# Optimization experiments

Hardware: AMD Instinct MI355X
Metric: run time of the kernel (lower is better)

The kernel has to match this reference:

```python
import jax, jax.numpy as jnp
import numpy as np

D_MODEL = 768
D_FF = 2048
N_EXP = 8
TOP_K = 2


def setup_inputs() -> dict:
    key = jax.random.key(0)
    ks = jax.random.split(key, 8)
    s = 0.02
    inputs = jax.random.normal(ks[0], (4, 2048, D_MODEL), dtype=jnp.float32)
    gate_w = jax.random.normal(ks[1], (D_MODEL, N_EXP), dtype=jnp.float32) * s
    w1 = jax.random.normal(ks[2], (N_EXP, D_MODEL, D_FF), dtype=jnp.float32) * s
    w3 = jax.random.normal(ks[3], (N_EXP, D_MODEL, D_FF), dtype=jnp.float32) * s
    w2 = jax.random.normal(ks[4], (N_EXP, D_FF, D_MODEL), dtype=jnp.float32) * s
    sw1 = jax.random.normal(ks[5], (D_MODEL, D_FF), dtype=jnp.float32) * s
    sw3 = jax.random.normal(ks[6], (D_MODEL, D_FF), dtype=jnp.float32) * s
    sw2 = jax.random.normal(ks[7], (D_FF, D_MODEL), dtype=jnp.float32) * s
    return {"inputs": inputs, "gate_w": gate_w, "w1": w1, "w3": w3, "w2": w2,
            "sw1": sw1, "sw3": sw3, "sw2": sw2}


def _swiglu(x, wa, wb, wc):
    # silu(x @ wa) * (x @ wb) @ wc
    return (jax.nn.silu(x @ wa) * (x @ wb)) @ wc


def reference(inputs, gate_w, w1, w3, w2, sw1, sw3, sw2):
    B, T, D = inputs.shape
    x = inputs.reshape(-1, D)                      # [N, D], N = B*T
    logits = x @ gate_w                            # [N, E]
    topk_scores, topk_idx = jax.lax.top_k(logits, TOP_K)  # [N, K]
    probs = jax.nn.softmax(topk_scores.astype(jnp.float32), axis=-1).astype(inputs.dtype)
    # per-token per-expert combine weight: [N, E]
    one_hot = jax.nn.one_hot(topk_idx, N_EXP, dtype=probs.dtype)  # [N, K, E]
    comb = jnp.einsum('nk,nke->ne', probs, one_hot)               # [N, E]
    out = jnp.zeros_like(x)
    for e in range(N_EXP):  # fixed small expert loop
        out = out + comb[:, e:e + 1] * _swiglu(x, w1[e], w3[e], w2[e])
    out = out + _swiglu(x, sw1, sw3, sw2)
    return out.reshape(B, T, D)
```

## Files before the change

### kernel.cpp

```cpp
#include <hip/hip_runtime.h>
#include <hip/hip_bf16.h>

#define N_TOK 8192
#define DM 768
#define DFF 2048
#define NE 8
#define SHARED_BASE 17408
#define TOTAL_ROWS 25600

typedef __attribute__((ext_vector_type(8))) __bf16 bf16x8;
typedef __attribute__((ext_vector_type(4))) float f32x4;

__device__ __forceinline__ unsigned short f2bf(float f) {
  union { float f; unsigned u; } a; a.f = f;
  unsigned r = a.u + 0x7FFFu + ((a.u >> 16) & 1u);
  return (unsigned short)(r >> 16);
}

__device__ __forceinline__ float bfu(unsigned short u) {
  union { unsigned u; float f; } x; x.u = (unsigned)u << 16; return x.f;
}

__device__ __forceinline__ void gload16(const void* g, void* l) {
  __builtin_amdgcn_global_load_lds((const __attribute__((address_space(1))) void*)g,
                                   (__attribute__((address_space(3))) void*)l, 16, 0, 0);
}


__global__ void transpose_all_kernel(
    const float* __restrict__ w1, const float* __restrict__ w3, const float* __restrict__ w2,
    const float* __restrict__ sw1, const float* __restrict__ sw3, const float* __restrict__ sw2,
    unsigned short* __restrict__ w1T, unsigned short* __restrict__ w3T,
    unsigned short* __restrict__ w2T,
    unsigned short* __restrict__ sw1T, unsigned short* __restrict__ sw3T,
    unsigned short* __restrict__ sw2T) {
  __shared__ float tile[64][65];
  const int z = blockIdx.z;
  const float* s; unsigned short* d; int R, C;
  if (z < 8)       { s = w1 + (size_t)z * DM * DFF;        d = w1T + (size_t)z * DM * DFF;        R = DM;  C = DFF; }
  else if (z < 16) { s = w3 + (size_t)(z - 8) * DM * DFF;  d = w3T + (size_t)(z - 8) * DM * DFF;  R = DM;  C = DFF; }
  else if (z < 24) { s = w2 + (size_t)(z - 16) * DFF * DM; d = w2T + (size_t)(z - 16) * DFF * DM; R = DFF; C = DM;  }
  else if (z == 24){ s = sw1; d = sw1T; R = DM;  C = DFF; }
  else if (z == 25){ s = sw3; d = sw3T; R = DM;  C = DFF; }
  else             { s = sw2; d = sw2T; R = DFF; C = DM;  }
  int c0 = blockIdx.x * 64, r0 = blockIdx.y * 64;
  if (c0 >= C || r0 >= R) return;
  int tx = threadIdx.x & 63, ty = threadIdx.x >> 6;
#pragma unroll
  for (int i = 0; i < 16; i++) {
    int row = i * 4 + ty;
    tile[row][tx] = s[(size_t)(r0 + row) * C + c0 + tx];
  }
  __syncthreads();
  int tx2 = threadIdx.x & 31, ty8 = threadIdx.x >> 5;
#pragma unroll
  for (int i = 0; i < 8; i++) {
    int row = i * 8 + ty8;
    ushort2 v;
    v.x = f2bf(tile[tx2 * 2][row]);
    v.y = f2bf(tile[tx2 * 2 + 1][row]);
    *(ushort2*)&d[(size_t)(c0 + row) * R + r0 + tx2 * 2] = v;
  }
}

__global__ __launch_bounds__(256) void gate_kernel(
    const float* __restrict__ x, const float* __restrict__ gw,
    float* __restrict__ probs, int* __restrict__ idxo, unsigned short* __restrict__ xb) {
  __shared__ float gws[8][768];
  const int tid = threadIdx.x;
  for (int i = tid; i < DM * 2; i += 256) {
    float4 v = ((const float4*)gw)[i];
    int dd = i >> 1;
    int e0 = (i & 1) * 4;
    gws[e0 + 0][dd] = v.x; gws[e0 + 1][dd] = v.y;
    gws[e0 + 2][dd] = v.z; gws[e0 + 3][dd] = v.w;
  }
  __syncthreads();
  const int lane = tid & 63, wv = tid >> 6;
  const int tok0 = blockIdx.x * 16 + wv * 4;
  for (int i = 0; i < 4; i++) {
    const int n = tok0 + i;
    const float* xr = x + (size_t)n * DM;
    float xv[12];
#pragma unroll
    for (int it = 0; it < 12; it++) xv[it] = xr[it * 64 + lane];
#pragma unroll
    for (int it = 0; it < 12; it++) xb[(size_t)n * DM + it * 64 + lane] = f2bf(xv[it]);
    double acc[8];
#pragma unroll
    for (int e = 0; e < 8; e++) {
      double a = 0.0;
#pragma unroll
      for (int it = 0; it < 12; it++) a += (double)xv[it] * (double)gws[e][it * 64 + lane];
      acc[e] = a;
    }
#pragma unroll
    for (int off = 32; off > 0; off >>= 1)
#pragma unroll
      for (int e = 0; e < 8; e++) acc[e] += __shfl_xor(acc[e], off);
    if (lane == 0) {
      int e0 = 0; double v0 = acc[0];
#pragma unroll
      for (int e = 1; e < 8; e++) if (acc[e] > v0) { v0 = acc[e]; e0 = e; }
      int e1 = -1; double v1 = -1e300;
#pragma unroll
      for (int e = 0; e < 8; e++) if (e != e0 && acc[e] > v1) { v1 = acc[e]; e1 = e; }
      double p0 = 1.0 / (1.0 + exp(v1 - v0));
      probs[n * 2 + 0] = (float)p0;
      probs[n * 2 + 1] = (float)(1.0 - p0);
      idxo[n * 2 + 0] = e0;
      idxo[n * 2 + 1] = e1;
    }
  }
}

__global__ __launch_bounds__(256) void route_kernel(
    const int* __restrict__ idxo,
    int* __restrict__ cnt, int* __restrict__ offs,
    int* __restrict__ list, int* __restrict__ slt) {
  __shared__ int lcnt[256][8];
  __shared__ int lstart[256][8];
  __shared__ int base[8];
  const int t = threadIdx.x;
#pragma unroll
  for (int e = 0; e < 8; e++) lcnt[t][e] = 0;
  __syncthreads();
  const int i0 = t * 64;
  for (int j = 0; j < 64; j++) {
    int e = idxo[i0 + j];
    lcnt[t][e]++;
  }
  __syncthreads();
  if (t < 8) {
    int run = 0;
    for (int tt = 0; tt < 256; tt++) { lstart[tt][t] = run; run += lcnt[tt][t]; }
    base[t] = run;
  }
  __syncthreads();
  if (t == 0) {
    int cum = 0;
    for (int e = 0; e < 8; e++) {
      int tot = base[e];
      cnt[e] = tot; offs[e] = cum;
      base[e] = cum;
      cum += (tot + 127) & ~127;
    }
    offs[8] = cum;
  }
  __syncthreads();
#pragma unroll
  for (int e = 0; e < 8; e++) lcnt[t][e] = base[e] + lstart[t][e];
  for (int j = 0; j < 64; j++) {
    int i = i0 + j;
    int e = idxo[i];
    int pos = lcnt[t][e]++;
    list[pos] = i >> 1;
    slt[i] = pos;
  }
}

__global__ __launch_bounds__(512, 4) void gemm1_kernel(
    const char* __restrict__ xb,
    const char* __restrict__ w1T,
    const char* __restrict__ w3T,
    const char* __restrict__ sw1T,
    const char* __restrict__ sw3T,
    const int* __restrict__ list, const int* __restrict__ cnt, const int* __restrict__ offs,
    unsigned short* __restrict__ Hb)
{
  __shared__ unsigned short Al[128 * 64];
  __shared__ unsigned short Bl[256 * 64];

  const int by = blockIdx.y;
  const int f0 = blockIdx.x * 128;
  const int tid = threadIdx.x;
  const int lane = tid & 63;
  const int wv = tid >> 6;
  const int wm = wv >> 2;
  const int wn = wv & 3;
  const int ml = lane & 15, kg = lane >> 4;

  const char *w1p, *w3p;
  int base_slot, tbase, cnt_e, offs_e = 0;
  const bool is_shared = (by >= 512);
  if (!is_shared) {
    int e = by >> 6, t = by & 63;
    cnt_e = cnt[e];
    if (t * 128 >= cnt_e) return;
    offs_e = offs[e];
    base_slot = offs_e + t * 128;
    tbase = t * 128;
    w1p = w1T + (size_t)e * DFF * DM * 2;
    w3p = w3T + (size_t)e * DFF * DM * 2;
  } else {
    int t = by - 512;
    base_slot = SHARED_BASE + t * 128;
    tbase = t * 128;
    cnt_e = 1 << 30;
    w1p = sw1T; w3p = sw3T;
  }

  const int srow = tid >> 3;
  const int schk = tid & 7;

  size_t abase[2];
#pragma unroll
  for (int it = 0; it < 2; it++) {
    int row = it * 64 + srow;
    int tok;
    if (is_shared) tok = tbase + row;
    else {
      int ie = tbase + row;
      if (ie >= cnt_e) ie = cnt_e - 1;
      tok = list[offs_e + ie];
    }
    abase[it] = (size_t)tok * (DM * 2) + (size_t)((schk ^ (row & 7)) << 4);
  }
  const char* bsrc[4];
#pragma unroll
  for (int it = 0; it < 4; it++) {
    int row = it * 64 + srow;
    int wn_r = row >> 6;
    int w = row & 63;
    int mat = w >> 5;
    int f = f0 + wn_r * 32 + (w & 31);
    bsrc[it] = (mat ? w3p : w1p) + (size_t)f * (DM * 2) + (size_t)((schk ^ (row & 7)) << 4);
  }

  f32x4 acc[4][4];
  const f32x4 z4 = {0.f, 0.f, 0.f, 0.f};
#pragma unroll
  for (int mi = 0; mi < 4; mi++)
#pragma unroll
    for (int nj = 0; nj < 4; nj++) acc[mi][nj] = z4;

  for (int ks = 0; ks < 12; ks++) {
#pragma unroll
    for (int it = 0; it < 2; it++)
      gload16(xb + abase[it] + ks * 128, (char*)Al + (size_t)((it * 512 + tid) * 16));
#pragma unroll
    for (int it = 0; it < 4; it++)
      gload16(bsrc[it] + ks * 128, (char*)Bl + (size_t)((it * 512 + tid) * 16));
    __syncthreads();
#pragma unroll
    for (int kk = 0; kk < 2; kk++) {
      const int kblk = kk * 4 + kg;
      const int chk = (kblk ^ (ml & 7)) << 4;
      bf16x8 af[4], bfr[4];
#pragma unroll
      for (int mi = 0; mi < 4; mi++) {
        int m = wm * 64 + mi * 16 + ml;
        af[mi] = *(const bf16x8*)((const char*)Al + m * 128 + chk);
      }
#pragma unroll
      for (int nj = 0; nj < 4; nj++) {
        int nn = wn * 64 + nj * 16 + ml;
        bfr[nj] = *(const bf16x8*)((const char*)Bl + nn * 128 + chk);
      }
#pragma unroll
      for (int mi = 0; mi < 4; mi++)
#pragma unroll
        for (int nj = 0; nj < 4; nj++)
          acc[mi][nj] = __builtin_amdgcn_mfma_f32_16x16x32_bf16(af[mi], bfr[nj], acc[mi][nj], 0, 0, 0);
    }
    __syncthreads();
  }

#pragma unroll
  for (int mi = 0; mi < 4; mi++) {
#pragma unroll
    for (int r = 0; r < 4; r++) {
      int row = wm * 64 + mi * 16 + (lane >> 4) * 4 + r;
      size_t hrow = (size_t)(base_slot + row) * DFF;
#pragma unroll
      for (int nj = 0; nj < 2; nj++) {
        float h1 = acc[mi][nj][r], h3 = acc[mi][nj + 2][r];
        float s = h1 / (1.0f + expf(-h1));
        Hb[hrow + f0 + wn * 32 + nj * 16 + ml] = f2bf(s * h3);
      }
    }
  }
}

__global__ __launch_bounds__(512, 4) void gemm2_kernel(
    const char* __restrict__ Hb,
    const char* __restrict__ w2T,
    const char* __restrict__ sw2T,
    const int* __restrict__ cnt, const int* __restrict__ offs,
    unsigned short* __restrict__ Obh,
    float* __restrict__ out)
{
  __shared__ unsigned short Al[128 * 64];
  __shared__ unsigned short Bl[256 * 64];

  const int by = blockIdx.y;
  const int d0 = blockIdx.x * 256;
  const int tid = threadIdx.x;
  const int lane = tid & 63;
  const int wv = tid >> 6;
  const int wm = wv >> 2;
  const int wn = wv & 3;
  const int ml = lane & 15, kg = lane >> 4;

  const char* w2p;
  int base_slot, tbase, cnt_e;
  const bool is_shared = (by >= 512);
  if (!is_shared) {
    int e = by >> 6, t = by & 63;
    cnt_e = cnt[e];
    if (t * 128 >= cnt_e) return;
    base_slot = offs[e] + t * 128;
    tbase = t * 128;
    w2p = w2T + (size_t)e * DM * DFF * 2;
  } else {
    int t = by - 512;
    base_slot = SHARED_BASE + t * 128;
    tbase = t * 128;
    cnt_e = 1 << 30;
    w2p = sw2T;
  }

  const int srow = tid >> 3, schk = tid & 7;
  size_t abase[2];
#pragma unroll
  for (int it = 0; it < 2; it++) {
    int row = it * 64 + srow;
    abase[it] = (size_t)(base_slot + row) * (DFF * 2) + (size_t)((schk ^ (row & 7)) << 4);
  }
  size_t bbase[4];
#pragma unroll
  for (int it = 0; it < 4; it++) {
    int row = it * 64 + srow;
    bbase[it] = (size_t)(d0 + row) * (DFF * 2) + (size_t)((schk ^ (row & 7)) << 4);
  }

  f32x4 acc[4][4];
  const f32x4 z4 = {0.f, 0.f, 0.f, 0.f};
#pragma unroll
  for (int mi = 0; mi < 4; mi++)
#pragma unroll
    for (int nj = 0; nj < 4; nj++) acc[mi][nj] = z4;

  for (int ks = 0; ks < 32; ks++) {
#pragma unroll
    for (int it = 0; it < 2; it++)
      gload16(Hb + abase[it] + ks * 128, (char*)Al + (size_t)((it * 512 + tid) * 16));
#pragma unroll
    for (int it = 0; it < 4; it++)
      gload16(w2p + bbase[it] + ks * 128, (char*)Bl + (size_t)((it * 512 + tid) * 16));
    __syncthreads();
#pragma unroll
    for (int kk = 0; kk < 2; kk++) {
      const int kblk = kk * 4 + kg;
      const int chk = (kblk ^ (ml & 7)) << 4;
      bf16x8 af[4], bfr[4];
#pragma unroll
      for (int mi = 0; mi < 4; mi++) {
        int m = wm * 64 + mi * 16 + ml;
        af[mi] = *(const bf16x8*)((const char*)Al + m * 128 + chk);
      }
#pragma unroll
      for (int nj = 0; nj < 4; nj++) {
        int nn = wn * 64 + nj * 16 + ml;
        bfr[nj] = *(const bf16x8*)((const char*)Bl + nn * 128 + chk);
      }
#pragma unroll
      for (int mi = 0; mi < 4; mi++)
#pragma unroll
        for (int nj = 0; nj < 4; nj++)
          acc[mi][nj] = __builtin_amdgcn_mfma_f32_16x16x32_bf16(af[mi], bfr[nj], acc[mi][nj], 0, 0, 0);
    }
    __syncthreads();
  }

#pragma unroll
  for (int mi = 0; mi < 4; mi++) {
#pragma unroll
    for (int r = 0; r < 4; r++) {
      int row = wm * 64 + mi * 16 + (lane >> 4) * 4 + r;
      if (is_shared) {
        float* orow = out + (size_t)(tbase + row) * DM + d0;
#pragma unroll
        for (int nj = 0; nj < 4; nj++)
          orow[wn * 64 + nj * 16 + ml] = acc[mi][nj][r];
      } else {
        unsigned short* orow = Obh + (size_t)(base_slot + row) * DM + d0;
#pragma unroll
        for (int nj = 0; nj < 4; nj++)
          orow[wn * 64 + nj * 16 + ml] = f2bf(acc[mi][nj][r]);
      }
    }
  }
}

__global__ __launch_bounds__(192) void combine_kernel(
    const unsigned short* __restrict__ Obh, const int* __restrict__ slt,
    const float* __restrict__ probs, float4* __restrict__ out4) {
  const int n = blockIdx.x;
  const int t = threadIdx.x;
  const int s0 = slt[2 * n], s1 = slt[2 * n + 1];
  const float p0 = probs[2 * n], p1 = probs[2 * n + 1];
  ushort4 b4 = *(const ushort4*)(Obh + (size_t)s0 * DM + t * 4);
  ushort4 c4 = *(const ushort4*)(Obh + (size_t)s1 * DM + t * 4);
  float4 a = out4[(size_t)n * 192 + t];
  a.x += p0 * bfu(b4.x) + p1 * bfu(c4.x);
  a.y += p0 * bfu(b4.y) + p1 * bfu(c4.y);
  a.z += p0 * bfu(b4.z) + p1 * bfu(c4.z);
  a.w += p0 * bfu(b4.w) + p1 * bfu(c4.w);
  out4[(size_t)n * 192 + t] = a;
}


extern "C" void kernel_launch(void* const* d_in, const int* in_sizes, int n_in,
                              void* d_out, int out_size, void* d_ws, size_t ws_size,
                              hipStream_t stream) {
  const float* x   = (const float*)d_in[0];
  const float* gw  = (const float*)d_in[1];
  const float* w1  = (const float*)d_in[2];
  const float* w3  = (const float*)d_in[3];
  const float* w2  = (const float*)d_in[4];
  const float* sw1 = (const float*)d_in[5];
  const float* sw3 = (const float*)d_in[6];
  const float* sw2 = (const float*)d_in[7];
  float* out = (float*)d_out;
  char* ws = (char*)d_ws;

  char* xb   = ws;
  char* w2T  = xb + 12582912;
  char* sw2T = w2T + 25165824;
  char* U    = sw2T + 3145728;
  char* w1T  = U;
  char* w3T  = w1T + 25165824;
  char* sw1T = w3T + 25165824;
  char* sw3T = sw1T + 3145728;
  char* Ob   = U;
  char* Hb   = U + 56623104;
  char* probs= Hb + 104857600;
  char* idxo = probs + 65536;
  char* lst  = idxo + 65536;
  char* slt  = lst + 69632;
  char* cntb = slt + 69632;
  char* offb = cntb + 64;

  transpose_all_kernel<<<dim3(32, 32, 27), 256, 0, stream>>>(
      w1, w3, w2, sw1, sw3, sw2,
      (unsigned short*)w1T, (unsigned short*)w3T, (unsigned short*)w2T,
      (unsigned short*)sw1T, (unsigned short*)sw3T, (unsigned short*)sw2T);

  gate_kernel<<<512, 256, 0, stream>>>(x, gw, (float*)probs, (int*)idxo, (unsigned short*)xb);
  route_kernel<<<1, 256, 0, stream>>>((const int*)idxo,
                                      (int*)cntb, (int*)offb, (int*)lst, (int*)slt);

  gemm1_kernel<<<dim3(16, 576), 512, 0, stream>>>(xb, w1T, w3T, sw1T, sw3T,
      (const int*)lst, (const int*)cntb, (const int*)offb, (unsigned short*)Hb);

  gemm2_kernel<<<dim3(3, 576), 512, 0, stream>>>(Hb, w2T, sw2T,
      (const int*)cntb, (const int*)offb, (unsigned short*)Ob, out);

  combine_kernel<<<N_TOK, 192, 0, stream>>>((const unsigned short*)Ob, (const int*)slt,
                                            (const float*)probs, (float4*)out);
}
```

Measured before the change: 395.4 us.

## Retile gemm1 into 256-thread blocks with separate w1/w3 tiles; trim transpose grid

The transpose launch shrinks from a 32x32 grid to 32x12, and the two block indices swap roles for the w2 matrices. This stops launching blocks that only checked bounds and returned. gemm1 changes from 512-thread blocks covering 128 FF columns to 256-thread blocks covering 64 FF columns, with separate LDS tiles and accumulators for w1 and w3, which doubles the grid width. The smaller tile gives more, lighter blocks, but each token tile is loaded from global memory twice as often.

Result: faster. 376.0 us (median of 3 runs) (-4.9%).

```diff
diff --git a/kernel.cpp b/kernel.cpp
--- a/kernel.cpp
+++ b/kernel.cpp
@@ -36,15 +36,15 @@
     unsigned short* __restrict__ sw2T) {
   __shared__ float tile[64][65];
   const int z = blockIdx.z;
-  const float* s; unsigned short* d; int R, C;
-  if (z < 8)       { s = w1 + (size_t)z * DM * DFF;        d = w1T + (size_t)z * DM * DFF;        R = DM;  C = DFF; }
-  else if (z < 16) { s = w3 + (size_t)(z - 8) * DM * DFF;  d = w3T + (size_t)(z - 8) * DM * DFF;  R = DM;  C = DFF; }
-  else if (z < 24) { s = w2 + (size_t)(z - 16) * DFF * DM; d = w2T + (size_t)(z - 16) * DFF * DM; R = DFF; C = DM;  }
-  else if (z == 24){ s = sw1; d = sw1T; R = DM;  C = DFF; }
-  else if (z == 25){ s = sw3; d = sw3T; R = DM;  C = DFF; }
-  else             { s = sw2; d = sw2T; R = DFF; C = DM;  }
-  int c0 = blockIdx.x * 64, r0 = blockIdx.y * 64;
-  if (c0 >= C || r0 >= R) return;
+  const float* s; unsigned short* d; int R, C; bool swapRC;
+  if (z < 8)       { s = w1 + (size_t)z * DM * DFF;        d = w1T + (size_t)z * DM * DFF;        R = DM;  C = DFF; swapRC = false; }
+  else if (z < 16) { s = w3 + (size_t)(z - 8) * DM * DFF;  d = w3T + (size_t)(z - 8) * DM * DFF;  R = DM;  C = DFF; swapRC = false; }
+  else if (z < 24) { s = w2 + (size_t)(z - 16) * DFF * DM; d = w2T + (size_t)(z - 16) * DFF * DM; R = DFF; C = DM;  swapRC = true;  }
+  else if (z == 24){ s = sw1; d = sw1T; R = DM;  C = DFF; swapRC = false; }
+  else if (z == 25){ s = sw3; d = sw3T; R = DM;  C = DFF; swapRC = false; }
+  else             { s = sw2; d = sw2T; R = DFF; C = DM;  swapRC = true;  }
+  int r0 = (swapRC ? blockIdx.x : blockIdx.y) * 64;
+  int c0 = (swapRC ? blockIdx.y : blockIdx.x) * 64;
   int tx = threadIdx.x & 63, ty = threadIdx.x >> 6;
 #pragma unroll
   for (int i = 0; i < 16; i++) {
@@ -159,7 +159,7 @@
   }
 }
 
-__global__ __launch_bounds__(512, 4) void gemm1_kernel(
+__global__ __launch_bounds__(256, 2) void gemm1_kernel(
     const char* __restrict__ xb,
     const char* __restrict__ w1T,
     const char* __restrict__ w3T,
@@ -169,16 +169,16 @@
     unsigned short* __restrict__ Hb)
 {
   __shared__ unsigned short Al[128 * 64];
-  __shared__ unsigned short Bl[256 * 64];
+  __shared__ unsigned short B1l[64 * 64];
+  __shared__ unsigned short B3l[64 * 64];
 
   const int by = blockIdx.y;
-  const int f0 = blockIdx.x * 128;
+  const int f0 = blockIdx.x * 64;
   const int tid = threadIdx.x;
   const int lane = tid & 63;
   const int wv = tid >> 6;
-  const int wm = wv >> 2;
-  const int wn = wv & 3;
-  const int ml = lane & 15, kg = lane >> 4;
+  const int wm = wv >> 1, wn = wv & 1;
+  const int wflat = tid & ~63;
 
   const char *w1p, *w3p;
   int base_slot, tbase, cnt_e, offs_e = 0;
@@ -200,13 +200,13 @@
     w1p = sw1T; w3p = sw3T;
   }
 
-  const int srow = tid >> 3;
-  const int schk = tid & 7;
-
-  size_t abase[2];
-#pragma unroll
-  for (int it = 0; it < 2; it++) {
-    int row = it * 64 + srow;
+  const int brow = tid >> 3;
+  const int bcol = tid & 7;
+
+  size_t abase[4];
+#pragma unroll
+  for (int it = 0; it < 4; it++) {
+    int row = it * 32 + brow;
     int tok;
     if (is_shared) tok = tbase + row;
     else {
@@ -214,54 +214,57 @@
       if (ie >= cnt_e) ie = cnt_e - 1;
       tok = list[offs_e + ie];
     }
-    abase[it] = (size_t)tok * (DM * 2) + (size_t)((schk ^ (row & 7)) << 4);
-  }
-  const char* bsrc[4];
-#pragma unroll
-  for (int it = 0; it < 4; it++) {
-    int row = it * 64 + srow;
-    int wn_r = row >> 6;
-    int w = row & 63;
-    int mat = w >> 5;
-    int f = f0 + wn_r * 32 + (w & 31);
-    bsrc[it] = (mat ? w3p : w1p) + (size_t)f * (DM * 2) + (size_t)((schk ^ (row & 7)) << 4);
-  }
-
-  f32x4 acc[4][4];
+    abase[it] = (size_t)tok * (DM * 2) + (size_t)((bcol ^ (row & 7)) << 4);
+  }
+  size_t bbase[2];
+#pragma unroll
+  for (int it = 0; it < 2; it++) {
+    int row = it * 32 + brow;
+    bbase[it] = (size_t)(f0 + row) * (DM * 2) + (size_t)((bcol ^ (row & 7)) << 4);
+  }
+
+  f32x4 acc1[4][2], acc3[4][2];
   const f32x4 z4 = {0.f, 0.f, 0.f, 0.f};
 #pragma unroll
   for (int mi = 0; mi < 4; mi++)
 #pragma unroll
-    for (int nj = 0; nj < 4; nj++) acc[mi][nj] = z4;
+    for (int ni = 0; ni < 2; ni++) { acc1[mi][ni] = z4; acc3[mi][ni] = z4; }
+
+  const int ml = lane & 15, kg = lane >> 4;
 
   for (int ks = 0; ks < 12; ks++) {
 #pragma unroll
-    for (int it = 0; it < 2; it++)
-      gload16(xb + abase[it] + ks * 128, (char*)Al + (size_t)((it * 512 + tid) * 16));
-#pragma unroll
     for (int it = 0; it < 4; it++)
-      gload16(bsrc[it] + ks * 128, (char*)Bl + (size_t)((it * 512 + tid) * 16));
+      gload16(xb + abase[it] + ks * 128, (char*)Al + (size_t)((it * 256 + wflat) * 16));
+#pragma unroll
+    for (int it = 0; it < 2; it++) {
+      gload16(w1p + bbase[it] + ks * 128, (char*)B1l + (size_t)((it * 256 + wflat) * 16));
+      gload16(w3p + bbase[it] + ks * 128, (char*)B3l + (size_t)((it * 256 + wflat) * 16));
+    }
     __syncthreads();
 #pragma unroll
     for (int kk = 0; kk < 2; kk++) {
       const int kblk = kk * 4 + kg;
-      const int chk = (kblk ^ (ml & 7)) << 4;
-      bf16x8 af[4], bfr[4];
+      bf16x8 af[4], b1f[2], b3f[2];
 #pragma unroll
       for (int mi = 0; mi < 4; mi++) {
         int m = wm * 64 + mi * 16 + ml;
-        af[mi] = *(const bf16x8*)((const char*)Al + m * 128 + chk);
-      }
-#pragma unroll
-      for (int nj = 0; nj < 4; nj++) {
-        int nn = wn * 64 + nj * 16 + ml;
-        bfr[nj] = *(const bf16x8*)((const char*)Bl + nn * 128 + chk);
+        af[mi] = *(const bf16x8*)((const char*)Al + m * 128 + ((kblk ^ (ml & 7)) << 4));
+      }
+#pragma unroll
+      for (int ni = 0; ni < 2; ni++) {
+        int nn = wn * 32 + ni * 16 + ml;
+        int boff = nn * 128 + ((kblk ^ (ml & 7)) << 4);
+        b1f[ni] = *(const bf16x8*)((const char*)B1l + boff);
+        b3f[ni] = *(const bf16x8*)((const char*)B3l + boff);
       }
 #pragma unroll
       for (int mi = 0; mi < 4; mi++)
 #pragma unroll
-        for (int nj = 0; nj < 4; nj++)
-          acc[mi][nj] = __builtin_amdgcn_mfma_f32_16x16x32_bf16(af[mi], bfr[nj], acc[mi][nj], 0, 0, 0);
+        for (int ni = 0; ni < 2; ni++) {
+          acc1[mi][ni] = __builtin_amdgcn_mfma_f32_16x16x32_bf16(af[mi], b1f[ni], acc1[mi][ni], 0, 0, 0);
+          acc3[mi][ni] = __builtin_amdgcn_mfma_f32_16x16x32_bf16(af[mi], b3f[ni], acc3[mi][ni], 0, 0, 0);
+        }
     }
     __syncthreads();
   }
@@ -269,14 +272,14 @@
 #pragma unroll
   for (int mi = 0; mi < 4; mi++) {
 #pragma unroll
-    for (int r = 0; r < 4; r++) {
-      int row = wm * 64 + mi * 16 + (lane >> 4) * 4 + r;
-      size_t hrow = (size_t)(base_slot + row) * DFF;
-#pragma unroll
-      for (int nj = 0; nj < 2; nj++) {
-        float h1 = acc[mi][nj][r], h3 = acc[mi][nj + 2][r];
+    for (int ni = 0; ni < 2; ni++) {
+#pragma unroll
+      for (int r = 0; r < 4; r++) {
+        int row = wm * 64 + mi * 16 + (lane >> 4) * 4 + r;
+        int col = f0 + wn * 32 + ni * 16 + ml;
+        float h1 = acc1[mi][ni][r], h3 = acc3[mi][ni][r];
         float s = h1 / (1.0f + expf(-h1));
-        Hb[hrow + f0 + wn * 32 + nj * 16 + ml] = f2bf(s * h3);
+        Hb[(size_t)(base_slot + row) * DFF + col] = f2bf(s * h3);
       }
     }
   }
@@ -442,7 +445,7 @@
   char* cntb = slt + 69632;
   char* offb = cntb + 64;
 
-  transpose_all_kernel<<<dim3(32, 32, 27), 256, 0, stream>>>(
+  transpose_all_kernel<<<dim3(32, 12, 27), 256, 0, stream>>>(
       w1, w3, w2, sw1, sw3, sw2,
       (unsigned short*)w1T, (unsigned short*)w3T, (unsigned short*)w2T,
       (unsigned short*)sw1T, (unsigned short*)sw3T, (unsigned short*)sw2T);
@@ -451,7 +454,7 @@
   route_kernel<<<1, 256, 0, stream>>>((const int*)idxo,
                                       (int*)cntb, (int*)offb, (int*)lst, (int*)slt);
 
-  gemm1_kernel<<<dim3(16, 576), 512, 0, stream>>>(xb, w1T, w3T, sw1T, sw3T,
+  gemm1_kernel<<<dim3(32, 576), 256, 0, stream>>>(xb, w1T, w3T, sw1T, sw3T,
       (const int*)lst, (const int*)cntb, (const int*)offb, (unsigned short*)Hb);
 
   gemm2_kernel<<<dim3(3, 576), 512, 0, stream>>>(Hb, w2T, sw2T,
```
